# Optimization experiments

Hardware: AMD Instinct MI355X
Metric: run time of the kernel (lower is better)

Reference implementation:

```python
import jax, jax.numpy as jnp
import numpy as np

N_NODES = 10000
N_EDGES = 160000
C_IN = 64      # in_irreps = 64x0e
C_TP = 16      # in_tp_irreps = 16x0e
C_KEY = 8      # key_irreps = (mul//2) = 8x0e
C_SH = 4       # spherical_harmonics_irreps = 4x0e
C_OTP = 16     # out_tp_irreps = 16x0e
C_OUT = 64     # out_irreps = 64x0e
EF = 32        # n_edge_features
FC = 128       # fc_dim (hardcoded in module)
W_NUMEL_K = C_TP * C_SH * C_KEY   # 512
W_NUMEL_V = C_TP * C_SH * C_OTP   # 1024
EPS = 1e-5


def _mlp(x, W1, b1, W2, b2, W3, b3):
    h = jax.nn.relu(x @ W1 + b1)
    h = jax.nn.relu(h @ W2 + b2)
    return h @ W3 + b3


def setup_inputs() -> dict:
    key = jax.random.key(0)
    ks = jax.random.split(key, 24)
    def nrm(k, shape, scale=1.0):
        return jax.random.normal(k, shape, dtype=jnp.float32) * scale
    inp = {}
    inp["node_data"] = nrm(ks[0], (N_NODES, C_IN))
    inp["edge_index"] = jax.random.randint(ks[1], (2, N_EDGES), 0, N_NODES, dtype=jnp.int32)
    inp["edge_data"] = nrm(ks[2], (N_EDGES, EF))
    inp["edge_sh"] = nrm(ks[3], (N_EDGES, C_SH))
    # e3nn Linear / TP internal weights (scalar-irrep specialization)
    inp["W_input"] = nrm(ks[4], (C_IN, C_TP))
    inp["W_query"] = nrm(ks[5], (C_TP, C_KEY))
    inp["W_dot"] = nrm(ks[6], (C_KEY, C_KEY))
    inp["W_output"] = nrm(ks[7], (C_OTP, C_OUT))
    # fc_key MLP: EF -> FC -> FC -> W_NUMEL_K
    inp["Wk1"] = nrm(ks[8], (EF, FC), 1.0 / np.sqrt(EF)); inp["bk1"] = jnp.zeros((FC,), jnp.float32)
    inp["Wk2"] = nrm(ks[9], (FC, FC), 1.0 / np.sqrt(FC)); inp["bk2"] = jnp.zeros((FC,), jnp.float32)
    inp["Wk3"] = nrm(ks[10], (FC, W_NUMEL_K), 1.0 / np.sqrt(FC)); inp["bk3"] = jnp.zeros((W_NUMEL_K,), jnp.float32)
    # fc_value MLP: EF -> FC -> FC -> W_NUMEL_V
    inp["Wv1"] = nrm(ks[11], (EF, FC), 1.0 / np.sqrt(EF)); inp["bv1"] = jnp.zeros((FC,), jnp.float32)
    inp["Wv2"] = nrm(ks[12], (FC, FC), 1.0 / np.sqrt(FC)); inp["bv2"] = jnp.zeros((FC,), jnp.float32)
    inp["Wv3"] = nrm(ks[13], (FC, W_NUMEL_V), 1.0 / np.sqrt(FC)); inp["bv3"] = jnp.zeros((W_NUMEL_V,), jnp.float32)
    inp["bn_weight"] = jnp.ones((C_OUT,), jnp.float32)
    inp["bn_bias"] = jnp.zeros((C_OUT,), jnp.float32)
    return inp


def reference(node_data, edge_index, edge_data, edge_sh,
              W_input, W_query, W_dot, W_output,
              Wk1, bk1, Wk2, bk2, Wk3, bk3,
              Wv1, bv1, Wv2, bv2, Wv3, bv3,
              bn_weight, bn_bias):
    N = node_data.shape[0]
    E = edge_data.shape[0]
    src, dst = edge_index[0], edge_index[1]

    # input_linear (e3nn Linear -> fan-in normalized matmul for scalar irreps)
    t = node_data @ W_input / np.sqrt(C_IN)          # [N, C_TP]
    q = t @ W_query / np.sqrt(C_TP)                  # [N, C_KEY]

    # dynamically generated per-edge TP weights
    wk = _mlp(edge_data, Wk1, bk1, Wk2, bk2, Wk3, bk3).reshape(E, C_TP, C_SH, C_KEY)
    wv = _mlp(edge_data, Wv1, bv1, Wv2, bv2, Wv3, bv3).reshape(E, C_TP, C_SH, C_OTP)

    ts = t[src]                                      # gather source node features [E, C_TP]
    # FullyConnectedTensorProduct on scalar irreps == per-edge weighted bilinear
    k = jnp.einsum('ea,es,easb->eb', ts, edge_sh, wk) / np.sqrt(C_TP * C_SH)   # [E, C_KEY]
    v = jnp.einsum('ea,es,easb->eb', ts, edge_sh, wv) / np.sqrt(C_TP * C_SH)   # [E, C_OTP]

    # dot(q[dest], k) -> scalar attention logit per edge
    a = (jnp.einsum('ea,eb,ab->e', q[dst], k, W_dot) / np.sqrt(C_KEY * C_KEY))[:, None]  # [E, 1]

    # segment softmax over edges grouped by destination node
    m = jax.ops.segment_max(a, dst, num_segments=N)
    m = jnp.where(jnp.isfinite(m), m, 0.0)           # empty segments -> 0 (matches scatter_max fill)
    a = jnp.exp(a - m[dst])
    z = jax.ops.segment_sum(a, dst, num_segments=N)
    a = a / z[dst]

    agg = jax.ops.segment_sum(a * v, dst, num_segments=N)   # [N, C_OTP]

    out = agg @ W_output / np.sqrt(C_OTP)            # [N, C_OUT]
    # residual: F.pad(node_data, (0, C_OUT - C_IN)); here C_OUT == C_IN so plain add
    out = out + node_data

    # e3nn BatchNorm on scalar irreps (training-mode batch stats, affine)
    mean = out.mean(axis=0)
    c = out - mean
    var = (c * c).mean(axis=0)
    out = c * jax.lax.rsqrt(var + EPS) * bn_weight + bn_bias
    return out
```

## Files before the change

kernel.cpp:

```cpp
#include <hip/hip_runtime.h>

#define N_NODES 10000
#define N_EDGES 160000

typedef unsigned short u16;
typedef unsigned int   u32;
typedef __bf16 bf16x8 __attribute__((ext_vector_type(8)));
typedef float  f32x4  __attribute__((ext_vector_type(4)));
typedef unsigned short u16x4 __attribute__((ext_vector_type(4)));

struct InP { const void* p[22]; };

static constexpr size_t WS_FLAG = 0;
static constexpr size_t WS_WIN  = 256;
static constexpr size_t WS_WQ   = WS_WIN  + 4096;
static constexpr size_t WS_WD   = WS_WQ   + 512;
static constexpr size_t WS_WOUT = WS_WD   + 256;
static constexpr size_t WS_BK1  = WS_WOUT + 4096;
static constexpr size_t WS_BK2  = WS_BK1  + 512;
static constexpr size_t WS_BK3  = WS_BK2  + 512;
static constexpr size_t WS_BV1  = WS_BK3  + 2048;
static constexpr size_t WS_BV2  = WS_BV1  + 512;
static constexpr size_t WS_BV3  = WS_BV2  + 512;
static constexpr size_t WS_BNW  = WS_BV3  + 4096;
static constexpr size_t WS_BNB  = WS_BNW  + 256;
static constexpr size_t WS_WK1T = WS_BNB  + 256;
static constexpr size_t WS_WK2T = WS_WK1T + 8192;
static constexpr size_t WS_WK3T = WS_WK2T + 32768;
static constexpr size_t WS_WV1T = WS_WK3T + 131072;
static constexpr size_t WS_WV2T = WS_WV1T + 8192;
static constexpr size_t WS_WV3T = WS_WV2T + 32768;
static constexpr size_t WS_T    = WS_WV3T + 262144;
static constexpr size_t WS_Q    = WS_T    + (size_t)N_NODES*16*4;
static constexpr size_t WS_Z    = WS_Q    + (size_t)N_NODES*8*4;
static constexpr size_t WS_AGG  = WS_Z    + (size_t)N_NODES*4;
static constexpr size_t WS_BNS  = WS_AGG  + (size_t)N_NODES*16*4;
static constexpr size_t WS_BNQ  = WS_BNS  + 256;
static constexpr size_t WS_OUTP = WS_BNQ  + 256;
static constexpr size_t ZERO_OFF = WS_Z;
static constexpr size_t ZERO_LEN = WS_OUTP - WS_Z;

__device__ __forceinline__ float loadf(const void* p, long i, int isbf){
  if(isbf){
    u32 x = ((u32)((const u16*)p)[i]) << 16;
    return __uint_as_float(x);
  }
  return ((const float*)p)[i];
}
__device__ __forceinline__ u16 f2b(float f){
  u32 u = __float_as_uint(f);
  u += 0x7fffu + ((u >> 16) & 1u);
  return (u16)(u >> 16);
}
__device__ __forceinline__ float b2f(u16 v){
  return __uint_as_float(((u32)v) << 16);
}
__device__ __forceinline__ bf16x8 ld8(const u16* p){
  uint4 v = *(const uint4*)p;
  return __builtin_bit_cast(bf16x8, v);
}

__global__ void k_detect(const void* edge_data, int* flag){
  int lane = threadIdx.x;
  u16 v = ((const u16*)edge_data)[lane*2];
  int ex = (v >> 7) & 0xFF;
  int sane = (ex >= 100 && ex <= 140) ? 1 : 0;
  unsigned long long b = __ballot(sane);
  if(lane == 0) flag[0] = (__popcll(b) >= 48) ? 1 : 0;
}

__global__ void k_convert(InP in, char* ws){
  const int isbf = *(const int*)(ws + WS_FLAG);
  long idx = (long)blockIdx.x*256 + threadIdx.x;
  const int    fsrc[12] = {4,5,6,7,9,11,13,15,17,19,20,21};
  const int    fcnt[12] = {1024,128,64,1024,128,128,512,128,128,1024,64,64};
  const size_t fdst[12] = {WS_WIN,WS_WQ,WS_WD,WS_WOUT,WS_BK1,WS_BK2,WS_BK3,WS_BV1,WS_BV2,WS_BV3,WS_BNW,WS_BNB};
  const long F_TOTAL = 4416;
  if(idx < F_TOTAL){
    long g = idx;
    for(int s=0;s<12;s++){
      if(g < fcnt[s]){ ((float*)(ws+fdst[s]))[g] = loadf(in.p[fsrc[s]], g, isbf); return; }
      g -= fcnt[s];
    }
    return;
  }
  long g = idx - F_TOTAL;
  const int    tsrc[6] = {8,10,12,14,16,18};
  const int    tK[6]   = {32,128,128,32,128,128};
  const int    tN[6]   = {128,128,512,128,128,1024};
  const size_t tdst[6] = {WS_WK1T,WS_WK2T,WS_WK3T,WS_WV1T,WS_WV2T,WS_WV3T};
  for(int s=0;s<6;s++){
    long cnt = (long)tK[s]*tN[s];
    if(g < cnt){
      int nk = tK[s] >> 5;
      int i = (int)(g & 7), ln = (int)((g>>3) & 63);
      int r2 = (int)(g >> 9);
      int kk = r2 % nk; int r3 = r2 / nk;
      int nt = r3 & 1;  int c  = r3 >> 1;
      int n = c*32 + nt*16 + (ln & 15);
      int k = kk*32 + (ln >> 4)*8 + i;
      ((u16*)(ws+tdst[s]))[g] = f2b(loadf(in.p[tsrc[s]], (long)k*tN[s] + n, isbf));
      return;
    }
    g -= cnt;
  }
}

__global__ void k_tq(InP in, char* ws){
  const int isbf = *(const int*)(ws + WS_FLAG);
  __shared__ float sWin[1024];
  __shared__ float sWq[128];
  __shared__ float sN[1024];
  __shared__ float sT[256];
  float* t_ws = (float*)(ws+WS_T);
  float* q_ws = (float*)(ws+WS_Q);
  int tid = threadIdx.x;
  for(int i=tid;i<1024;i+=256) sWin[i] = ((const float*)(ws+WS_WIN))[i];
  if(tid<128) sWq[tid] = ((const float*)(ws+WS_WQ))[tid];
  int n0 = blockIdx.x*16;
  for(int i=tid;i<1024;i+=256) sN[i] = loadf(in.p[0], (long)n0*64 + i, isbf);
  __syncthreads();
  int ni = tid>>4, j = tid&15;
  float acc = 0.f;
  #pragma unroll 8
  for(int i=0;i<64;i++) acc += sN[ni*64+i]*sWin[i*16+j];
  float t = acc*0.125f;
  t_ws[(n0+ni)*16+j] = t;
  sT[tid] = t;
  __syncthreads();
  if(tid<128){
    int n2 = tid>>3, b = tid&7;
    float a2 = 0.f;
    #pragma unroll
    for(int jj=0;jj<16;jj++) a2 += sT[n2*16+jj]*sWq[jj*8+b];
    q_ws[(n0+n2)*8+b] = a2*0.25f;
  }
}

__global__ __launch_bounds__(256,3) void k_edges(InP in, char* ws){
  const int isbf = *(const int*)(ws + WS_FLAG);
  const int* ei = (const int*)in.p[1];
  const float* t_ws = (const float*)(ws + WS_T);
  const float* q_ws = (const float*)(ws + WS_Q);
  float* Zp  = (float*)(ws + WS_Z);
  float* AGG = (float*)(ws + WS_AGG);

  __shared__ __align__(16) char smem[51200];
  u16*   sED = (u16*)smem;
  u16*   sH1 = (u16*)(smem + 4096);
  u16*   sH2 = (u16*)(smem + 20480);
  u16*   sPT = (u16*)(smem + 36864);
  float* sK  = (float*)(smem + 45056);
  float* sV  = (float*)(smem + 47104);
  float* sP  = (float*)smem;
  int*   sDst= (int*)(smem + 256);

  const int tid  = threadIdx.x;
  const int e0   = blockIdx.x * 64;
  const int lane = tid & 63, wv = tid >> 6;
  const int lrow = lane & 15, lquad = lane >> 4;

  {
    int e = tid >> 2, q4 = tid & 3;
    u16 tmp[8];
    if(isbf){
      uint4 vv = *(const uint4*)((const u16*)in.p[2] + (long)(e0+e)*32 + q4*8);
      *(uint4*)tmp = vv;
    } else {
      const float* fp = (const float*)in.p[2] + (long)(e0+e)*32 + q4*8;
      f32x4 a = *(const f32x4*)fp, b = *(const f32x4*)(fp+4);
      #pragma unroll
      for(int r=0;r<4;r++){ tmp[r]=f2b(a[r]); tmp[4+r]=f2b(b[r]); }
    }
    *(uint4*)&sED[(e>>4)*512 + (q4*16 + (e&15))*8] = *(uint4*)tmp;
  }
  {
    int e = tid >> 2, j4 = tid & 3;
    int src = ei[e0+e];
    *(f32x4*)&sV[e*16 + j4*4] = *(const f32x4*)&t_ws[src*16 + j4*4];
  }
  {
    int e = tid >> 2, s4 = tid & 3;
    sK[tid] = loadf(in.p[3], (long)(e0+e)*4 + s4, isbf);
  }
  float qreg[8]; int mydst = 0;
  if(wv == 0){
    mydst = ei[N_EDGES + e0 + lane];
    #pragma unroll
    for(int a=0;a<8;a++) qreg[a] = q_ws[mydst*8 + a];
  }
  __syncthreads();
  for(int idx = tid; idx < 4096; idx += 256){
    int e = idx & 63, as = idx >> 6;
    sPT[as*64 + e] = f2b(sV[e*16 + (as>>2)] * sK[e*4 + (as&3)]);
  }
  __syncthreads();
  for(int idx = tid; idx < 1536; idx += 256) sK[idx] = 0.f;

  auto dense = [&](const u16* A, int ts, int nkL, const u16* Wg, const float* biasg, u16* O){
    bf16x8 bw[2][4]; f32x4 bb[2];
    for(int nt=0;nt<2;nt++){
      for(int kk=0;kk<nkL;kk++)
        bw[nt][kk] = ld8(&Wg[(((wv*2+nt)*nkL + kk)<<9) + lane*8]);
      bb[nt] = *(const f32x4*)&biasg[wv*32 + nt*16 + lquad*4];
    }
    for(int et=0;et<4;et++){
      bf16x8 af[4];
      for(int kk=0;kk<nkL;kk++) af[kk] = ld8(&A[et*ts + (kk<<9) + lane*8]);
      for(int nt=0;nt<2;nt++){
        f32x4 c = {0.f,0.f,0.f,0.f};
        for(int kk=0;kk<nkL;kk++)
          c = __builtin_amdgcn_mfma_f32_16x16x32_bf16(bw[nt][kk], af[kk], c, 0, 0, 0);
        u16x4 pk;
        #pragma unroll
        for(int r=0;r<4;r++){
          float h = c[r] + bb[nt][r];
          h = h > 0.f ? h : 0.f;
          pk[r] = f2b(h);
        }
        int off = et*2048 + (wv<<9) + (nt*2 + (lquad>>1))*128 + lrow*8 + (lquad&1)*4;
        *(u16x4*)&O[off] = pk;
      }
    }
  };

  auto matvec = [&](const u16* Wg, const float* biasg, int NJ, int isval){
    float kp[16];
    #pragma unroll
    for(int i=0;i<16;i++) kp[i]=0.f;
    const int c0 = wv*NJ;
    bf16x8 bw[2][2][4]; f32x4 bb[2][2];
    #pragma unroll
    for(int nt=0;nt<2;nt++){
      #pragma unroll
      for(int kk=0;kk<4;kk++)
        bw[0][nt][kk] = ld8(&Wg[(((c0*2+nt)*4 + kk)<<9) + lane*8]);
      bb[0][nt] = *(const f32x4*)&biasg[c0*32 + nt*16 + lquad*4];
    }
    #pragma unroll
    for(int j=0;j<NJ;j++){
      int cur = j&1, nxt = cur^1;
      if(j+1 < NJ){
        int cn = c0 + j + 1;
        #pragma unroll
        for(int nt=0;nt<2;nt++){
          #pragma unroll
          for(int kk=0;kk<4;kk++)
            bw[nxt][nt][kk] = ld8(&Wg[(((cn*2+nt)*4 + kk)<<9) + lane*8]);
          bb[nxt][nt] = *(const f32x4*)&biasg[cn*32 + nt*16 + lquad*4];
        }
      }
      for(int et=0;et<4;et++){
        bf16x8 af[4];
        #pragma unroll
        for(int kk=0;kk<4;kk++)
          af[kk] = ld8(&sH2[et*2048 + (kk<<9) + lane*8]);
        const int e = et*16 + lrow;
        for(int nt=0;nt<2;nt++){
          f32x4 c = {0.f,0.f,0.f,0.f};
          #pragma unroll
          for(int kk=0;kk<4;kk++)
            c = __builtin_amdgcn_mfma_f32_16x16x32_bf16(bw[cur][nt][kk], af[kk], c, 0, 0, 0);
          int n0 = (c0+j)*32 + nt*16 + lquad*4;
          int as = isval ? (n0>>4) : (n0>>3);
          float pv = b2f(sPT[as*64 + e]);
          #pragma unroll
          for(int r=0;r<4;r++)
            kp[et*4+r] += pv * (c[r] + bb[cur][nt][r]);
        }
      }
    }
    if(isval){
      for(int et=0;et<4;et++){
        int e = et*16 + lrow;
        #pragma unroll
        for(int r=0;r<4;r++)
          atomicAdd(&sV[e*16 + lquad*4 + r], kp[et*4+r]*0.125f);
      }
    } else {
      int b0 = (lquad & 1)*4;
      for(int et=0;et<4;et++){
        int e = et*16 + lrow;
        #pragma unroll
        for(int r=0;r<4;r++)
          atomicAdd(&sK[e*8 + b0 + r], kp[et*4+r]*0.125f);
      }
    }
  };

  dense(sED, 512, 1, (const u16*)(ws+WS_WK1T), (const float*)(ws+WS_BK1), sH1); __syncthreads();
  dense(sH1, 2048,4, (const u16*)(ws+WS_WK2T), (const float*)(ws+WS_BK2), sH2); __syncthreads();
  matvec((const u16*)(ws+WS_WK3T), (const float*)(ws+WS_BK3), 4, 0);
  dense(sED, 512, 1, (const u16*)(ws+WS_WV1T), (const float*)(ws+WS_BV1), sH1); __syncthreads();
  dense(sH1, 2048,4, (const u16*)(ws+WS_WV2T), (const float*)(ws+WS_BV2), sH2); __syncthreads();
  matvec((const u16*)(ws+WS_WV3T), (const float*)(ws+WS_BV3), 8, 1);            __syncthreads();

  if(wv == 0){
    const float* wdf = (const float*)(ws + WS_WD);
    float acc = 0.f;
    #pragma unroll
    for(int a=0;a<8;a++){
      float qa = qreg[a];
      #pragma unroll
      for(int b=0;b<8;b++)
        acc += qa * wdf[a*8+b] * sK[lane*8+b];
    }
    float p = __expf(acc * 0.125f);
    atomicAdd(Zp + mydst, p);
    sP[lane] = p;
    sDst[lane] = mydst;
  }
  __syncthreads();
  for(int idx = tid; idx < 1024; idx += 256){
    int e = idx >> 4;
    atomicAdd(AGG + (long)sDst[e]*16 + (idx & 15), sP[e]*sV[idx]);
  }
}

__global__ void k7a(InP in, char* ws){
  const int isbf = *(const int*)(ws + WS_FLAG);
  __shared__ float sWo[1024];
  __shared__ float ls[256], lq[256];
  int tid = threadIdx.x;
  for(int i=tid;i<1024;i+=256) sWo[i] = ((const float*)(ws+WS_WOUT))[i];
  __syncthreads();
  const float* AGG = (const float*)(ws+WS_AGG);
  const float* Zp  = (const float*)(ws+WS_Z);
  float* OUTP = (float*)(ws+WS_OUTP);
  int c = tid & 63, r4 = tid >> 6;
  float s=0.f, q=0.f;
  for(int it=0; it<20; it++){
    int n = blockIdx.x*80 + it*4 + r4;
    float z = Zp[n];
    float inv = z > 0.f ? 0.25f/z : 0.f;
    const float* ag = AGG + (long)n*16;
    float acc = 0.f;
    #pragma unroll
    for(int j=0;j<16;j++) acc += ag[j]*sWo[j*64+c];
    float o = acc*inv + loadf(in.p[0], (long)n*64 + c, isbf);
    OUTP[(long)n*64+c] = o;
    s += o; q += o*o;
  }
  ls[tid]=s; lq[tid]=q;
  __syncthreads();
  if(tid < 64){
    float ss = ls[tid]+ls[tid+64]+ls[tid+128]+ls[tid+192];
    float qq = lq[tid]+lq[tid+64]+lq[tid+128]+lq[tid+192];
    atomicAdd((float*)(ws+WS_BNS)+tid, ss);
    atomicAdd((float*)(ws+WS_BNQ)+tid, qq);
  }
}

__global__ void k7c(char* ws, void* d_out){
  const int isbf = *(const int*)(ws + WS_FLAG);
  int idx = blockIdx.x*256 + threadIdx.x;
  if(idx >= N_NODES*64) return;
  int c = idx & 63;
  float s  = ((const float*)(ws+WS_BNS))[c];
  float qq = ((const float*)(ws+WS_BNQ))[c];
  float mean = s * (1.f/N_NODES);
  float var  = qq * (1.f/N_NODES) - mean*mean;
  float sc = rsqrtf(var + 1e-5f) * ((const float*)(ws+WS_BNW))[c];
  float val = (((const float*)(ws+WS_OUTP))[idx] - mean)*sc + ((const float*)(ws+WS_BNB))[c];
  if(isbf) ((u16*)d_out)[idx] = f2b(val);
  else     ((float*)d_out)[idx] = val;
}

extern "C" void kernel_launch(void* const* d_in, const int* in_sizes, int n_in,
                              void* d_out, int out_size, void* d_ws, size_t ws_size,
                              hipStream_t stream){
  InP in;
  for(int i=0;i<22;i++) in.p[i] = d_in[i];
  char* ws = (char*)d_ws;

  hipMemsetAsync(ws + ZERO_OFF, 0, ZERO_LEN, stream);
  k_detect<<<1,64,0,stream>>>((const void*)d_in[2], (int*)(ws+WS_FLAG));
  k_convert<<<946,256,0,stream>>>(in, ws);
  k_tq<<<625,256,0,stream>>>(in, ws);
  k_edges<<<2500,256,0,stream>>>(in, ws);
  k7a<<<125,256,0,stream>>>(in, ws);
  k7c<<<2500,256,0,stream>>>(ws, d_out);
}
```

Baseline: 322.8 us.

## Fuse MLP layers 2 and 3 via register shuffles, split layer 3 over K

Layer 2 output no longer goes through shared memory. It is repacked in registers with cross-lane shuffles so it can feed straight into the layer-3 MFMA as its operand. Layer 3 is now split across waves along the reduction dimension (each wave owns one K slice and loops over all output columns), and the partial products are combined with shared-memory atomics. This drops the sH2 buffer, shrinking LDS from 51200 to 34816 bytes, and removes one barrier per MLP. The bias is folded into the MFMA accumulator init. The cost is more shuffle instructions and reading the full W3 in every wave.

```diff
diff --git a/kernel.cpp b/kernel.cpp
--- a/kernel.cpp
+++ b/kernel.cpp
@@ -137,6 +137,134 @@
   }
 }
 
+
+__device__ __forceinline__ void dense1(int wv, int lane, int lquad, int lrow,
+                                       const u16* __restrict__ Wg,
+                                       const float* __restrict__ biasg,
+                                       const u16* sED, u16* sH1){
+  bf16x8 bw0 = ld8(&Wg[((wv*2+0)<<9) + lane*8]);
+  bf16x8 bw1 = ld8(&Wg[((wv*2+1)<<9) + lane*8]);
+  f32x4 bb0 = *(const f32x4*)&biasg[wv*32 +  0 + lquad*4];
+  f32x4 bb1 = *(const f32x4*)&biasg[wv*32 + 16 + lquad*4];
+  #pragma unroll
+  for(int et=0;et<4;et++){
+    bf16x8 a = ld8(&sED[et*512 + lane*8]);
+    f32x4 c0 = __builtin_amdgcn_mfma_f32_16x16x32_bf16(bw0, a, bb0, 0, 0, 0);
+    f32x4 c1 = __builtin_amdgcn_mfma_f32_16x16x32_bf16(bw1, a, bb1, 0, 0, 0);
+    u16x4 pk0, pk1;
+    #pragma unroll
+    for(int r=0;r<4;r++){
+      float h0 = c0[r] > 0.f ? c0[r] : 0.f; pk0[r] = f2b(h0);
+      float h1 = c1[r] > 0.f ? c1[r] : 0.f; pk1[r] = f2b(h1);
+    }
+    int base = et*2048 + (wv<<9) + (lquad>>1)*128 + lrow*8 + (lquad&1)*4;
+    *(u16x4*)&sH1[base      ] = pk0;
+    *(u16x4*)&sH1[base + 256] = pk1;
+  }
+}
+
+template<int NC, int ISVAL>
+__device__ __forceinline__ void l23(int wv, int lane, int lquad, int lrow,
+                                    const u16* __restrict__ W2, const float* __restrict__ b2,
+                                    const u16* __restrict__ W3, const float* __restrict__ b3,
+                                    const u16* sH1, const u16* sPT, float* sKV){
+  const int hi = lane >> 5;
+  const int s0 = ((lane>>4)&1)*32 + (lane&15);
+
+  bf16x8 w20 = ld8(&W2[(((wv*2+0)*4+0)<<9) + lane*8]);
+  bf16x8 w21 = ld8(&W2[(((wv*2+0)*4+1)<<9) + lane*8]);
+  bf16x8 w22 = ld8(&W2[(((wv*2+0)*4+2)<<9) + lane*8]);
+  bf16x8 w23 = ld8(&W2[(((wv*2+0)*4+3)<<9) + lane*8]);
+  bf16x8 w24 = ld8(&W2[(((wv*2+1)*4+0)<<9) + lane*8]);
+  bf16x8 w25 = ld8(&W2[(((wv*2+1)*4+1)<<9) + lane*8]);
+  bf16x8 w26 = ld8(&W2[(((wv*2+1)*4+2)<<9) + lane*8]);
+  bf16x8 w27 = ld8(&W2[(((wv*2+1)*4+3)<<9) + lane*8]);
+  f32x4 bb20 = *(const f32x4*)&b2[wv*32 +  0 + lquad*4];
+  f32x4 bb21 = *(const f32x4*)&b2[wv*32 + 16 + lquad*4];
+
+  bf16x8 af0, af1, af2, af3;
+#define D2_ET(ET, AF) { \
+    bf16x8 a0 = ld8(&sH1[ET*2048 + (0<<9) + lane*8]); \
+    bf16x8 a1 = ld8(&sH1[ET*2048 + (1<<9) + lane*8]); \
+    bf16x8 a2 = ld8(&sH1[ET*2048 + (2<<9) + lane*8]); \
+    bf16x8 a3 = ld8(&sH1[ET*2048 + (3<<9) + lane*8]); \
+    f32x4 c0 = bb20, c1 = bb21; \
+    c0 = __builtin_amdgcn_mfma_f32_16x16x32_bf16(w20, a0, c0, 0, 0, 0); \
+    c0 = __builtin_amdgcn_mfma_f32_16x16x32_bf16(w21, a1, c0, 0, 0, 0); \
+    c0 = __builtin_amdgcn_mfma_f32_16x16x32_bf16(w22, a2, c0, 0, 0, 0); \
+    c0 = __builtin_amdgcn_mfma_f32_16x16x32_bf16(w23, a3, c0, 0, 0, 0); \
+    c1 = __builtin_amdgcn_mfma_f32_16x16x32_bf16(w24, a0, c1, 0, 0, 0); \
+    c1 = __builtin_amdgcn_mfma_f32_16x16x32_bf16(w25, a1, c1, 0, 0, 0); \
+    c1 = __builtin_amdgcn_mfma_f32_16x16x32_bf16(w26, a2, c1, 0, 0, 0); \
+    c1 = __builtin_amdgcn_mfma_f32_16x16x32_bf16(w27, a3, c1, 0, 0, 0); \
+    float h0 = c0[0]>0.f?c0[0]:0.f, h1 = c0[1]>0.f?c0[1]:0.f; \
+    float h2 = c0[2]>0.f?c0[2]:0.f, h3 = c0[3]>0.f?c0[3]:0.f; \
+    u32 p00 = ((u32)f2b(h1)<<16) | (u32)f2b(h0); \
+    u32 p01 = ((u32)f2b(h3)<<16) | (u32)f2b(h2); \
+    h0 = c1[0]>0.f?c1[0]:0.f; h1 = c1[1]>0.f?c1[1]:0.f; \
+    h2 = c1[2]>0.f?c1[2]:0.f; h3 = c1[3]>0.f?c1[3]:0.f; \
+    u32 p10 = ((u32)f2b(h1)<<16) | (u32)f2b(h0); \
+    u32 p11 = ((u32)f2b(h3)<<16) | (u32)f2b(h2); \
+    int a00 = __shfl((int)p00, s0),    a01 = __shfl((int)p01, s0); \
+    int a10 = __shfl((int)p10, s0),    a11 = __shfl((int)p11, s0); \
+    int b00 = __shfl((int)p00, s0+16), b01 = __shfl((int)p01, s0+16); \
+    int b10 = __shfl((int)p10, s0+16), b11 = __shfl((int)p11, s0+16); \
+    uint4 uv; \
+    uv.x = (u32)(hi ? a10 : a00); \
+    uv.y = (u32)(hi ? a11 : a01); \
+    uv.z = (u32)(hi ? b10 : b00); \
+    uv.w = (u32)(hi ? b11 : b01); \
+    AF = __builtin_bit_cast(bf16x8, uv); }
+  D2_ET(0, af0)
+  D2_ET(1, af1)
+  D2_ET(2, af2)
+  D2_ET(3, af3)
+#undef D2_ET
+
+  f32x4 kp0 = {0.f,0.f,0.f,0.f}, kp1 = {0.f,0.f,0.f,0.f};
+  f32x4 kp2 = {0.f,0.f,0.f,0.f}, kp3 = {0.f,0.f,0.f,0.f};
+#define MV_ET(ET, AF, KP) { \
+      const int e = ET*16 + lrow; \
+      f32x4 c0 = __builtin_amdgcn_mfma_f32_16x16x32_bf16(w30, AF, bb30, 0, 0, 0); \
+      f32x4 c1 = __builtin_amdgcn_mfma_f32_16x16x32_bf16(w31, AF, bb31, 0, 0, 0); \
+      const int n00 = j*32 +  0 + lquad*4; \
+      const int n01 = j*32 + 16 + lquad*4; \
+      const int as0 = ISVAL ? (n00>>4) : (n00>>3); \
+      const int as1 = ISVAL ? (n01>>4) : (n01>>3); \
+      const float pv0 = b2f(sPT[as0*64 + e]); \
+      const float pv1 = b2f(sPT[as1*64 + e]); \
+      KP += c0*pv0 + c1*pv1; }
+  #pragma unroll 2
+  for(int j=0;j<NC;j++){
+    bf16x8 w30 = ld8(&W3[(((j*2+0)*4 + wv)<<9) + lane*8]);
+    bf16x8 w31 = ld8(&W3[(((j*2+1)*4 + wv)<<9) + lane*8]);
+    f32x4 bb30 = {0.f,0.f,0.f,0.f}, bb31 = {0.f,0.f,0.f,0.f};
+    if(wv == 0){
+      bb30 = *(const f32x4*)&b3[j*32 +  0 + lquad*4];
+      bb31 = *(const f32x4*)&b3[j*32 + 16 + lquad*4];
+    }
+    MV_ET(0, af0, kp0)
+    MV_ET(1, af1, kp1)
+    MV_ET(2, af2, kp2)
+    MV_ET(3, af3, kp3)
+  }
+#undef MV_ET
+
+  const int b0     = ISVAL ? (lquad*4) : ((lquad&1)*4);
+  const int stride = ISVAL ? 16 : 8;
+#define ST_ET(ET, KP) { \
+    const int e = ET*16 + lrow; \
+    atomicAdd(&sKV[e*stride + b0 + 0], KP[0]*0.125f); \
+    atomicAdd(&sKV[e*stride + b0 + 1], KP[1]*0.125f); \
+    atomicAdd(&sKV[e*stride + b0 + 2], KP[2]*0.125f); \
+    atomicAdd(&sKV[e*stride + b0 + 3], KP[3]*0.125f); }
+  ST_ET(0, kp0)
+  ST_ET(1, kp1)
+  ST_ET(2, kp2)
+  ST_ET(3, kp3)
+#undef ST_ET
+}
+
 __global__ __launch_bounds__(256,3) void k_edges(InP in, char* ws){
   const int isbf = *(const int*)(ws + WS_FLAG);
   const int* ei = (const int*)in.p[1];
@@ -145,13 +273,12 @@
   float* Zp  = (float*)(ws + WS_Z);
   float* AGG = (float*)(ws + WS_AGG);
 
-  __shared__ __align__(16) char smem[51200];
+  __shared__ __align__(16) char smem[34816];
   u16*   sED = (u16*)smem;
   u16*   sH1 = (u16*)(smem + 4096);
-  u16*   sH2 = (u16*)(smem + 20480);
-  u16*   sPT = (u16*)(smem + 36864);
-  float* sK  = (float*)(smem + 45056);
-  float* sV  = (float*)(smem + 47104);
+  u16*   sPT = (u16*)(smem + 20480);
+  float* sK  = (float*)(smem + 28672);
+  float* sV  = (float*)(smem + 30720);
   float* sP  = (float*)smem;
   int*   sDst= (int*)(smem + 256);
 
@@ -197,103 +324,18 @@
   __syncthreads();
   for(int idx = tid; idx < 1536; idx += 256) sK[idx] = 0.f;
 
-  auto dense = [&](const u16* A, int ts, int nkL, const u16* Wg, const float* biasg, u16* O){
-    bf16x8 bw[2][4]; f32x4 bb[2];
-    for(int nt=0;nt<2;nt++){
-      for(int kk=0;kk<nkL;kk++)
-        bw[nt][kk] = ld8(&Wg[(((wv*2+nt)*nkL + kk)<<9) + lane*8]);
-      bb[nt] = *(const f32x4*)&biasg[wv*32 + nt*16 + lquad*4];
-    }
-    for(int et=0;et<4;et++){
-      bf16x8 af[4];
-      for(int kk=0;kk<nkL;kk++) af[kk] = ld8(&A[et*ts + (kk<<9) + lane*8]);
-      for(int nt=0;nt<2;nt++){
-        f32x4 c = {0.f,0.f,0.f,0.f};
-        for(int kk=0;kk<nkL;kk++)
-          c = __builtin_amdgcn_mfma_f32_16x16x32_bf16(bw[nt][kk], af[kk], c, 0, 0, 0);
-        u16x4 pk;
-        #pragma unroll
-        for(int r=0;r<4;r++){
-          float h = c[r] + bb[nt][r];
-          h = h > 0.f ? h : 0.f;
-          pk[r] = f2b(h);
-        }
-        int off = et*2048 + (wv<<9) + (nt*2 + (lquad>>1))*128 + lrow*8 + (lquad&1)*4;
-        *(u16x4*)&O[off] = pk;
-      }
-    }
-  };
-
-  auto matvec = [&](const u16* Wg, const float* biasg, int NJ, int isval){
-    float kp[16];
-    #pragma unroll
-    for(int i=0;i<16;i++) kp[i]=0.f;
-    const int c0 = wv*NJ;
-    bf16x8 bw[2][2][4]; f32x4 bb[2][2];
-    #pragma unroll
-    for(int nt=0;nt<2;nt++){
-      #pragma unroll
-      for(int kk=0;kk<4;kk++)
-        bw[0][nt][kk] = ld8(&Wg[(((c0*2+nt)*4 + kk)<<9) + lane*8]);
-      bb[0][nt] = *(const f32x4*)&biasg[c0*32 + nt*16 + lquad*4];
-    }
-    #pragma unroll
-    for(int j=0;j<NJ;j++){
-      int cur = j&1, nxt = cur^1;
-      if(j+1 < NJ){
-        int cn = c0 + j + 1;
-        #pragma unroll
-        for(int nt=0;nt<2;nt++){
-          #pragma unroll
-          for(int kk=0;kk<4;kk++)
-            bw[nxt][nt][kk] = ld8(&Wg[(((cn*2+nt)*4 + kk)<<9) + lane*8]);
-          bb[nxt][nt] = *(const f32x4*)&biasg[cn*32 + nt*16 + lquad*4];
-        }
-      }
-      for(int et=0;et<4;et++){
-        bf16x8 af[4];
-        #pragma unroll
-        for(int kk=0;kk<4;kk++)
-          af[kk] = ld8(&sH2[et*2048 + (kk<<9) + lane*8]);
-        const int e = et*16 + lrow;
-        for(int nt=0;nt<2;nt++){
-          f32x4 c = {0.f,0.f,0.f,0.f};
-          #pragma unroll
-          for(int kk=0;kk<4;kk++)
-            c = __builtin_amdgcn_mfma_f32_16x16x32_bf16(bw[cur][nt][kk], af[kk], c, 0, 0, 0);
-          int n0 = (c0+j)*32 + nt*16 + lquad*4;
-          int as = isval ? (n0>>4) : (n0>>3);
-          float pv = b2f(sPT[as*64 + e]);
-          #pragma unroll
-          for(int r=0;r<4;r++)
-            kp[et*4+r] += pv * (c[r] + bb[cur][nt][r]);
-        }
-      }
-    }
-    if(isval){
-      for(int et=0;et<4;et++){
-        int e = et*16 + lrow;
-        #pragma unroll
-        for(int r=0;r<4;r++)
-          atomicAdd(&sV[e*16 + lquad*4 + r], kp[et*4+r]*0.125f);
-      }
-    } else {
-      int b0 = (lquad & 1)*4;
-      for(int et=0;et<4;et++){
-        int e = et*16 + lrow;
-        #pragma unroll
-        for(int r=0;r<4;r++)
-          atomicAdd(&sK[e*8 + b0 + r], kp[et*4+r]*0.125f);
-      }
-    }
-  };
-
-  dense(sED, 512, 1, (const u16*)(ws+WS_WK1T), (const float*)(ws+WS_BK1), sH1); __syncthreads();
-  dense(sH1, 2048,4, (const u16*)(ws+WS_WK2T), (const float*)(ws+WS_BK2), sH2); __syncthreads();
-  matvec((const u16*)(ws+WS_WK3T), (const float*)(ws+WS_BK3), 4, 0);
-  dense(sED, 512, 1, (const u16*)(ws+WS_WV1T), (const float*)(ws+WS_BV1), sH1); __syncthreads();
-  dense(sH1, 2048,4, (const u16*)(ws+WS_WV2T), (const float*)(ws+WS_BV2), sH2); __syncthreads();
-  matvec((const u16*)(ws+WS_WV3T), (const float*)(ws+WS_BV3), 8, 1);            __syncthreads();
+  dense1(wv, lane, lquad, lrow, (const u16*)(ws+WS_WK1T), (const float*)(ws+WS_BK1), sED, sH1);
+  __syncthreads();
+  l23<16,0>(wv, lane, lquad, lrow,
+            (const u16*)(ws+WS_WK2T), (const float*)(ws+WS_BK2),
+            (const u16*)(ws+WS_WK3T), (const float*)(ws+WS_BK3), sH1, sPT, sK);
+  __syncthreads();
+  dense1(wv, lane, lquad, lrow, (const u16*)(ws+WS_WV1T), (const float*)(ws+WS_BV1), sED, sH1);
+  __syncthreads();
+  l23<32,1>(wv, lane, lquad, lrow,
+            (const u16*)(ws+WS_WV2T), (const float*)(ws+WS_BV2),
+            (const u16*)(ws+WS_WV3T), (const float*)(ws+WS_BV3), sH1, sPT, sV);
+  __syncthreads();
 
   if(wv == 0){
     const float* wdf = (const float*)(ws + WS_WD);
```

Measured after the change: 328.1 us. No clear change (+1.6%).
